# Optimization experiments

Measured on AMD Instinct MI355X. Metric: run time of the kernel, lower is better.

## Reference

```python
import jax, jax.numpy as jnp
import numpy as np

B, T, F = 256, 2048, 20
H_NODES = 256


def _heaviside(x):
    # smooth heaviside approx used throughout the original module
    return (jnp.tanh(10.0 * x) + 1.0) * 0.5


def _evap(wu, wl, wd, pet):
    h = _heaviside
    et1 = h(wu - pet) * pet + h(pet - wu) * wu
    rp = h(pet - et1) * (pet - et1)  # h(-(pet-et1))*0 term vanishes
    et22 = h(rp - wl) * wl + h(wl - rp) * rp
    et2 = h(rp) * et22
    et33 = h(rp - et2 - wd) * wd + h(wd - (rp - et2)) * (rp - et2)
    et3 = h(rp - et2) * et33
    return et1, et2, et3


def _runoff(wu, wl, wd, p, wum, wlm, wdm, b, c):
    wum = wum * 19.9 + 0.1
    wlm = wlm * 30.0 + 60.0
    wdm = wdm * 60.0 + 60.0
    c = c * 0.19 + 0.01
    b = b * 0.3 + 0.1
    w_total = wum + wlm + wdm
    s = c * (wu / w_total) ** 2 + b * (wl / w_total) ** 2
    return _heaviside(p - s) * (p - s)


def _partition(runoff, k1, k2, k3):
    k1 = k1 * 0.69 + 0.01
    k2 = k2 * 0.69 + 0.01
    k3 = k3 * 0.89 + 0.01
    sr = k1 * runoff
    itf = k2 * (runoff - sr)
    bf = k3 * (runoff - sr - itf)
    return sr, itf, bf


def setup_inputs() -> dict:
    key = jax.random.key(0)
    ks = jax.random.split(key, 7)
    u = lambda k, shp: jax.random.uniform(k, shp, jnp.float32, -0.05, 0.05)
    inputs = jax.random.uniform(ks[0], (B, T, F), jnp.float32)
    return {
        "inputs": inputs,
        "w1": u(ks[1], (15, H_NODES)),
        "b1": jnp.zeros((H_NODES,), jnp.float32),
        "w2": u(ks[2], (H_NODES, 64)),
        "b2": jnp.zeros((64,), jnp.float32),
        "w3": u(ks[3], (64, 8)),
        "b3": jnp.zeros((8,), jnp.float32),
    }


def reference(inputs, w1, b1, w2, b2, w3, b3):
    pet = inputs[..., 0:1]
    tmean = inputs[..., 1:2]
    p = inputs[..., 2:3]
    attrs = inputs[..., 5:]  # [B,T,15]

    # static-attribute -> physical-parameter MLP
    h1 = jnp.tanh(attrs @ w1 + b1)
    h2 = jnp.tanh(h1 @ w2 + b2)
    params = jax.nn.sigmoid(h2 @ w3 + b3)  # [B,T,8]

    xs = jnp.concatenate([pet, p, tmean, params], axis=-1)  # [B,T,11]

    def step(state, x):
        wu, wl, wd = state[:, 0:1], state[:, 1:2], state[:, 2:3]
        pet_t, p_t = x[:, 0:1], x[:, 1:2]
        et1, et2, et3 = _evap(wu, wl, wd, pet_t)
        clip = lambda d: jnp.clip(d, -1e5, 1e5)
        wu_n = wu + clip(p_t - et1)
        wl_n = wl + clip(p_t - et1 - et2)
        wd_n = wd + clip(p_t - et1 - et2 - et3)
        ns = jnp.concatenate([wu_n, wl_n, wd_n], axis=1)  # [B,3]
        return ns, ns

    init = jnp.zeros((inputs.shape[0], 3), inputs.dtype)
    _, outs = jax.lax.scan(step, init, jnp.swapaxes(xs, 0, 1))  # [T,B,3]
    outputs = jnp.swapaxes(outs, 0, 1)  # [B,T,3]

    wu, wl, wd = outputs[..., 0:1], outputs[..., 1:2], outputs[..., 2:3]
    wum, wlm, wdm = params[..., 0:1], params[..., 1:2], params[..., 2:3]
    b, c = params[..., 3:4], params[..., 4:5]
    k1, k2, k3 = params[..., 5:6], params[..., 6:7], params[..., 7:8]

    et1, et2, et3 = _evap(wu, wl, wd, pet)
    # NOTE: original call() swaps (wl,wd) and (wlm,wdm) here - kept faithful
    runoff = _runoff(wu, wd, wl, p, wum, wdm, wlm, b, c)
    sr, itf, bf = _partition(runoff, k1, k2, k3)
    total_q = sr + itf * 0.5 + bf * 0.25  # flow routing
    return total_q  # [B,T,1]
```

## Files before the change

### kernel.cpp

```cpp
#include <hip/hip_runtime.h>

#define B_ 256
#define T_ 2048
#define F_ 20
#define NT (B_*T_)
#define CH 16
#define NCH (T_/CH)

typedef __bf16 bf16x8 __attribute__((ext_vector_type(8)));
typedef float  f32x4  __attribute__((ext_vector_type(4)));

__device__ __forceinline__ float ex2(float x){ return __builtin_amdgcn_exp2f(x); }
__device__ __forceinline__ float rcpf_(float x){ return __builtin_amdgcn_rcpf(x); }

#define K10F 28.853900817779268f
#define K1F   2.8853900817779268f
#define LOG2E 1.4426950408889634f

__device__ __forceinline__ float hside(float x){ return 1.0f - rcpf_(ex2(K10F*x) + 1.0f); }
__device__ __forceinline__ float tanh_f(float z){ return 1.0f - 2.0f*rcpf_(ex2(K1F*z) + 1.0f); }
__device__ __forceinline__ float sigmoid_f(float z){ return rcpf_(1.0f + ex2(-LOG2E*z)); }


__global__ __launch_bounds__(256) void prep_kernel(const float* __restrict__ in,
                                                   float* __restrict__ ws){
  int r = blockIdx.x*256 + threadIdx.x;
  if (r >= NT) return;
  int b = r & (B_-1);
  int t = r >> 8;
  const float* src = in + ((size_t)b*T_ + t)*F_;
  ((float2*)ws)[r] = make_float2(src[0], src[2]);
}

__global__ __launch_bounds__(512) void fused_kernel(const float* __restrict__ in,
    const float* __restrict__ w1, const float* __restrict__ b1,
    const float* __restrict__ w2, const float* __restrict__ b2,
    const float* __restrict__ w3, const float* __restrict__ b3,
    float* __restrict__ ws){
  extern __shared__ char sm[];
  float* params = ws + 4*(size_t)NT;

  if (blockIdx.x < 4) {
    const float2* pp2 = (const float2*)ws;
    float* wuT = ws + 2*(size_t)NT;
    float* wdT = ws + 3*(size_t)NT;
    float*  d1L = (float*)sm;
    float*  bsQ = (float*)(sm + 8192);
    float2* rhL = (float2*)(sm + 24576);
    float2* qbL = (float2*)(sm + 40960);

    int tid = threadIdx.x;
    int wv = tid >> 6, lane = tid & 63;
    int boff = blockIdx.x * 64;

    float wu = 0.0f, wl = 0.0f, wd = 0.0f;
    float2 buf[2][8];

    if (wv == 0){
      #pragma unroll
      for (int g = 0; g < 2; ++g)
        #pragma unroll
        for (int i = 0; i < 8; ++i)
          buf[g][i] = pp2[(g*8 + i)*B_ + boff + lane];
    }

    for (int it = 0; it < NCH + 3; ++it){
      if (wv == 0){
        if (it < NCH){
          int c = it, par = c & 1;
          #pragma unroll
          for (int g = 0; g < 2; ++g){
            #pragma unroll
            for (int i = 0; i < 8; ++i){
              int s = g*8 + i;
              float pet = buf[g][i].x, p = buf[g][i].y;
              float d  = wu - pet;
              float r1 = rcpf_(ex2(K10F*d) + 1.0f);
              float d1 = -d*r1;
              float base = (p - pet) + d1;
              wu += base;
              wuT[(c*CH + s)*B_ + boff + lane] = wu;
              d1L[par*(CH*64) + s*64 + lane] = d1;
              bsQ[(c&3)*(CH*64) + s*64 + lane] = base;
            }
            int cn = (c + 1 < NCH) ? c + 1 : c;
            #pragma unroll
            for (int i = 0; i < 8; ++i)
              buf[g][i] = pp2[(cn*CH + g*8 + i)*B_ + boff + lane];
          }
        }
      } else if (wv == 1){
        if (it >= 1 && it <= NCH){
          int c = it - 1, par = c & 1;
          #pragma unroll
          for (int s = 0; s < CH; ++s){
            float d1 = d1L[par*(CH*64) + s*64 + lane];
            float r2 = rcpf_(ex2(K10F*d1) + 1.0f);
            float rp = fmaf(-d1, r2, d1);
            float hrp = 1.0f - rcpf_(ex2(K10F*rp) + 1.0f);
            rhL[par*(CH*64) + s*64 + lane] = make_float2(rp, hrp);
          }
        }
      } else if (wv == 2){
        if (it >= 2 && it <= NCH + 1){
          int c = it - 2, par = c & 1;
          #pragma unroll
          for (int s = 0; s < CH; ++s){
            float2 rh  = rhL[par*(CH*64) + s*64 + lane];
            float base = bsQ[(c&3)*(CH*64) + s*64 + lane];
            float d2   = rh.x - wl;
            float r    = rcpf_(ex2(K10F*d2) + 1.0f);
            float et22 = fmaf(d2, r, wl);
            float et2  = rh.y * et22;
            float b2   = base - et2;
            wl += b2;
            qbL[par*(CH*64) + s*64 + lane] = make_float2(rh.x - et2, b2);
          }
        }
      } else if (wv == 3){
        if (it >= 3){
          int c = it - 3, par = c & 1;
          #pragma unroll
          for (int s = 0; s < CH; ++s){
            float2 qb  = qbL[par*(CH*64) + s*64 + lane];
            float hqv  = 1.0f - rcpf_(ex2(K10F*qb.x) + 1.0f);
            float d3   = qb.x - wd;
            float r    = rcpf_(ex2(K10F*d3) + 1.0f);
            float et33 = fmaf(d3, r, wd);
            float et3  = hqv * et33;
            wd += qb.y - et3;
            wdT[(c*CH + s)*B_ + boff + lane] = wd;
          }
        }
      }
      __syncthreads();
    }
    return;
  }

  __bf16* w1f  = (__bf16*)sm;
  __bf16* w2f  = (__bf16*)(sm + 8192);
  float*  b1s  = (float*)(sm + 40960);
  float*  b2s  = (float*)(sm + 41984);
  float*  w3s  = (float*)(sm + 42240);
  float*  b3s  = (float*)(sm + 44288);
  __bf16* hbufA= (__bf16*)(sm + 44320);

  int tid = threadIdx.x;

  for (int s = tid; s < 16*32*8; s += 512) w1f[s] = (__bf16)0.0f;
  __syncthreads();
  for (int idx = tid; idx < 15*256; idx += 512){
    int k = idx >> 8, n = idx & 255;
    int ct = n >> 4;
    int l  = ((k>>3)*16) + (n & 15);
    int j  = k & 7;
    w1f[(ct*32 + l)*8 + j] = (__bf16)w1[idx];
  }
  for (int idx = tid; idx < 256*64; idx += 512){
    int k = idx >> 6, n = idx & 63;
    int kb = k >> 5;
    int lq = (k >> 3) & 3;
    int j  = k & 7;
    int ct = n >> 4;
    int l  = lq*16 + (n & 15);
    w2f[((kb*4 + ct)*64 + l)*8 + j] = (__bf16)w2[idx];
  }
  if (tid < 256) b1s[tid] = b1[tid];
  if (tid < 64)  b2s[tid] = b2[tid];
  if (tid < 512) w3s[tid] = w3[tid];
  if (tid < 8)   b3s[tid] = b3[tid];
  __syncthreads();

  int lane = tid & 63;
  int wv   = tid >> 6;
  int m    = lane & 15;
  int q    = lane >> 4;
  int r0   = (blockIdx.x - 4)*128 + wv*16;

  int rowA = r0 + m;
  int bA = rowA & (B_-1), tA = rowA >> 8;
  const float* ap = in + ((size_t)bA*T_ + tA)*F_ + 5;
  bf16x8 a1;
  #pragma unroll
  for (int j = 0; j < 8; ++j){
    int k = q*8 + j;
    float v = (k < 15) ? ap[k] : 0.0f;
    a1[j] = (__bf16)v;
  }

  __bf16* hb = hbufA + wv*1152;
  f32x4 zero4 = {0.0f, 0.0f, 0.0f, 0.0f};
  bf16x8 zero8;
  #pragma unroll
  for (int j = 0; j < 8; ++j) zero8[j] = (__bf16)0.0f;

  f32x4 acc2[4] = {zero4, zero4, zero4, zero4};

  #pragma unroll
  for (int p = 0; p < 4; ++p){
    #pragma unroll
    for (int c4 = 0; c4 < 4; ++c4){
      int ct = p*4 + c4;
      bf16x8 bw = zero8;
      if (lane < 32) bw = *(const bf16x8*)&w1f[(ct*32 + lane)*8];
      f32x4 c1 = __builtin_amdgcn_mfma_f32_16x16x32_bf16(a1, bw, zero4, 0, 0, 0);
      int f = c4*16 + m;
      float bb = b1s[p*64 + f];
      #pragma unroll
      for (int i = 0; i < 4; ++i){
        float h = tanh_f(c1[i] + bb);
        hb[(q*4 + i)*72 + f] = (__bf16)h;
      }
    }
    #pragma unroll
    for (int kb = 0; kb < 2; ++kb){
      bf16x8 a2 = *(const bf16x8*)&hb[m*72 + q*8 + kb*32];
      #pragma unroll
      for (int ct = 0; ct < 4; ++ct){
        bf16x8 bw2 = *(const bf16x8*)&w2f[(((p*2 + kb)*4 + ct)*64 + lane)*8];
        acc2[ct] = __builtin_amdgcn_mfma_f32_16x16x32_bf16(a2, bw2, acc2[ct], 0, 0, 0);
      }
    }
  }

  #pragma unroll
  for (int ct = 0; ct < 4; ++ct){
    int f = ct*16 + m;
    float bb = b2s[f];
    #pragma unroll
    for (int i = 0; i < 4; ++i){
      float h = tanh_f(acc2[ct][i] + bb);
      hb[(q*4 + i)*72 + f] = (__bf16)h;
    }
  }

  float z0 = b3s[2*q], z1 = b3s[2*q + 1];
  #pragma unroll
  for (int kb3 = 0; kb3 < 8; ++kb3){
    bf16x8 hv8 = *(const bf16x8*)&hb[m*72 + kb3*8];
    #pragma unroll
    for (int j = 0; j < 8; ++j){
      float hv = (float)hv8[j];
      int k = kb3*8 + j;
      z0 = fmaf(hv, w3s[k*8 + 2*q],     z0);
      z1 = fmaf(hv, w3s[k*8 + 2*q + 1], z1);
    }
  }
  int rowO = r0 + m;
  float2 outp = make_float2(sigmoid_f(z0), sigmoid_f(z1));
  *(float2*)&params[(size_t)rowO*8 + 2*q] = outp;
}

__global__ __launch_bounds__(256) void final_kernel(const float* __restrict__ ws,
                                                    float* __restrict__ out){
  int r = blockIdx.x*256 + threadIdx.x;
  if (r >= NT) return;
  const float2* pp2 = (const float2*)ws;
  const float* wuT  = ws + 2*(size_t)NT;
  const float* wdT  = ws + 3*(size_t)NT;
  const float* params = ws + 4*(size_t)NT;

  float p  = pp2[r].y;
  float wu = wuT[r], wd = wdT[r];
  const float4* pp = (const float4*)(params + (size_t)r*8);
  float4 p0 = pp[0], p1 = pp[1];
  float wum   = fmaf(p0.x, 19.9f, 0.1f);
  float wlm_s = fmaf(p0.z, 30.0f, 60.0f);
  float wdm_s = fmaf(p0.y, 60.0f, 60.0f);
  float cc = fmaf(p1.x, 0.19f, 0.01f);
  float bb = fmaf(p0.w, 0.30f, 0.10f);
  float wt = wum + wlm_s + wdm_s;
  float xu = wu / wt;
  float xd = wd / wt;
  float s  = cc*xu*xu + bb*xd*xd;
  float ps = p - s;
  float runoff = hside(ps)*ps;
  float k1p = fmaf(p1.y, 0.69f, 0.01f);
  float k2p = fmaf(p1.z, 0.69f, 0.01f);
  float k3p = fmaf(p1.w, 0.89f, 0.01f);
  float sr  = k1p*runoff;
  float itf = k2p*(runoff - sr);
  float bf  = k3p*(runoff - sr - itf);
  int b = r & (B_-1);
  int t = r >> 8;
  out[(size_t)b*T_ + t] = sr + 0.5f*itf + 0.25f*bf;
}

extern "C" void kernel_launch(void* const* d_in, const int* in_sizes, int n_in,
                              void* d_out, int out_size, void* d_ws, size_t ws_size,
                              hipStream_t stream) {
  const float* in = (const float*)d_in[0];
  const float* w1 = (const float*)d_in[1];
  const float* b1 = (const float*)d_in[2];
  const float* w2 = (const float*)d_in[3];
  const float* b2 = (const float*)d_in[4];
  const float* w3 = (const float*)d_in[5];
  const float* b3 = (const float*)d_in[6];
  float* out = (float*)d_out;
  float* ws  = (float*)d_ws;

  prep_kernel <<<NT/256,      256, 0,     stream>>>(in, ws);
  fused_kernel<<<NT/128 + 4,  512, 62752, stream>>>(in, w1, b1, w2, b2, w3, b3, ws);
  final_kernel<<<NT/256,      256, 0,     stream>>>(ws, out);
}
```

Before: 220.9 us.

## Split scan across more blocks, prescale state, offload loads/stores to helper waves

The serial scan now runs on 8 blocks of 32 lanes instead of 4 blocks of 64. Its state is kept pre-scaled by the tanh constant, which removes the multiply before each exp2. Global loads of the next chunk and global stores of wu/wd move to two extra helper waves that use shared-memory double buffers, so the latency-critical recurrence waves touch only LDS. The final kernel gains an LDS tile transpose so output stores are coalesced. The cost is half-empty wavefronts and an extra pipeline stage of latency.

```diff
diff --git a/kernel.cpp b/kernel.cpp
--- a/kernel.cpp
+++ b/kernel.cpp
@@ -14,6 +14,7 @@
 __device__ __forceinline__ float rcpf_(float x){ return __builtin_amdgcn_rcpf(x); }
 
 #define K10F 28.853900817779268f
+#define INVK 0.034657359027997264f
 #define K1F   2.8853900817779268f
 #define LOG2E 1.4426950408889634f
 
@@ -40,97 +41,130 @@
   extern __shared__ char sm[];
   float* params = ws + 4*(size_t)NT;
 
-  if (blockIdx.x < 4) {
+  if (blockIdx.x < 8) {
     const float2* pp2 = (const float2*)ws;
     float* wuT = ws + 2*(size_t)NT;
     float* wdT = ws + 3*(size_t)NT;
-    float*  d1L = (float*)sm;
-    float*  bsQ = (float*)(sm + 8192);
-    float2* rhL = (float2*)(sm + 24576);
-    float2* qbL = (float2*)(sm + 40960);
-
-    int tid = threadIdx.x;
-    int wv = tid >> 6, lane = tid & 63;
-    int boff = blockIdx.x * 64;
-
-    float wu = 0.0f, wl = 0.0f, wd = 0.0f;
-    float2 buf[2][8];
-
-    if (wv == 0){
+    float2* ppL = (float2*)sm;
+    float2* dkb = (float2*)(sm + 8192);
+    float2* rhb = (float2*)(sm + 16384);
+    float2* qbb = (float2*)(sm + 24576);
+    float*  bb2 = (float*)(sm + 32768);
+    float*  wub = (float*)(sm + 36864);
+    float*  wdb = (float*)(sm + 40960);
+
+    int tid  = threadIdx.x;
+    int wv   = tid >> 6;
+    int l64  = tid & 63;
+    bool act = l64 < 32;
+    int lane = l64 & 31;
+    int boff = blockIdx.x * 32;
+
+    float Wu = 0.0f, WL = 0.0f, WD = 0.0f;
+
+    if (wv == 4 && act){
+      float2 v[CH];
       #pragma unroll
-      for (int g = 0; g < 2; ++g)
-        #pragma unroll
-        for (int i = 0; i < 8; ++i)
-          buf[g][i] = pp2[(g*8 + i)*B_ + boff + lane];
-    }
-
-    for (int it = 0; it < NCH + 3; ++it){
+      for (int s = 0; s < CH; ++s) v[s] = pp2[s*B_ + boff + lane];
+      #pragma unroll
+      for (int s = 0; s < CH; ++s)
+        ppL[s*32 + lane] = make_float2(K10F*v[s].x, K10F*(v[s].y - v[s].x));
+    }
+    __syncthreads();
+
+    for (int it = 0; it < NCH + 4; ++it){
       if (wv == 0){
-        if (it < NCH){
-          int c = it, par = c & 1;
-          #pragma unroll
-          for (int g = 0; g < 2; ++g){
-            #pragma unroll
-            for (int i = 0; i < 8; ++i){
-              int s = g*8 + i;
-              float pet = buf[g][i].x, p = buf[g][i].y;
-              float d  = wu - pet;
-              float r1 = rcpf_(ex2(K10F*d) + 1.0f);
-              float d1 = -d*r1;
-              float base = (p - pet) + d1;
-              wu += base;
-              wuT[(c*CH + s)*B_ + boff + lane] = wu;
-              d1L[par*(CH*64) + s*64 + lane] = d1;
-              bsQ[(c&3)*(CH*64) + s*64 + lane] = base;
-            }
-            int cn = (c + 1 < NCH) ? c + 1 : c;
-            #pragma unroll
-            for (int i = 0; i < 8; ++i)
-              buf[g][i] = pp2[(cn*CH + g*8 + i)*B_ + boff + lane];
+        int c = it;
+        if (c < NCH && act){
+          int par = c & 1;
+          #pragma unroll
+          for (int s = 0; s < CH; ++s){
+            float2 pe = ppL[(par*CH + s)*32 + lane];
+            float t1  = Wu - pe.x;
+            float r   = rcpf_(ex2(t1) + 1.0f);
+            float WuPP= Wu + pe.y;
+            float Wn  = fmaf(-t1, r, WuPP);
+            float dK  = -t1*r;
+            float BASE= pe.y + dK;
+            dkb[(par*CH + s)*32 + lane] = make_float2(dK, BASE);
+            wub[(par*CH + s)*32 + lane] = Wn;
+            Wu = Wn;
           }
         }
       } else if (wv == 1){
-        if (it >= 1 && it <= NCH){
-          int c = it - 1, par = c & 1;
+        int c = it - 1;
+        if (c >= 0 && c < NCH && act){
+          int par = c & 1;
           #pragma unroll
           for (int s = 0; s < CH; ++s){
-            float d1 = d1L[par*(CH*64) + s*64 + lane];
-            float r2 = rcpf_(ex2(K10F*d1) + 1.0f);
-            float rp = fmaf(-d1, r2, d1);
-            float hrp = 1.0f - rcpf_(ex2(K10F*rp) + 1.0f);
-            rhL[par*(CH*64) + s*64 + lane] = make_float2(rp, hrp);
+            float2 db = dkb[(par*CH + s)*32 + lane];
+            float r1  = rcpf_(ex2(db.x) + 1.0f);
+            float RP  = fmaf(-db.x, r1, db.x);
+            float HRP = 1.0f - rcpf_(ex2(RP) + 1.0f);
+            rhb[(par*CH + s)*32 + lane] = make_float2(RP, HRP);
+            bb2[(par*CH + s)*32 + lane] = db.y;
           }
         }
       } else if (wv == 2){
-        if (it >= 2 && it <= NCH + 1){
-          int c = it - 2, par = c & 1;
+        int c = it - 2;
+        if (c >= 0 && c < NCH && act){
+          int par = c & 1;
           #pragma unroll
           for (int s = 0; s < CH; ++s){
-            float2 rh  = rhL[par*(CH*64) + s*64 + lane];
-            float base = bsQ[(c&3)*(CH*64) + s*64 + lane];
-            float d2   = rh.x - wl;
-            float r    = rcpf_(ex2(K10F*d2) + 1.0f);
-            float et22 = fmaf(d2, r, wl);
-            float et2  = rh.y * et22;
-            float b2   = base - et2;
-            wl += b2;
-            qbL[par*(CH*64) + s*64 + lane] = make_float2(rh.x - et2, b2);
+            float2 rh  = rhb[(par*CH + s)*32 + lane];
+            float BASE = bb2[(par*CH + s)*32 + lane];
+            float D2   = rh.x - WL;
+            float r    = rcpf_(ex2(D2) + 1.0f);
+            float et22 = fmaf(D2, r, WL);
+            float WLB  = WL + BASE;
+            float Wn   = fmaf(-rh.y, et22, WLB);
+            float ET2  = rh.y * et22;
+            qbb[(par*CH + s)*32 + lane] = make_float2(rh.x - ET2, BASE - ET2);
+            WL = Wn;
           }
         }
       } else if (wv == 3){
-        if (it >= 3){
-          int c = it - 3, par = c & 1;
+        int c = it - 3;
+        if (c >= 0 && c < NCH && act){
+          int par = c & 1;
           #pragma unroll
           for (int s = 0; s < CH; ++s){
-            float2 qb  = qbL[par*(CH*64) + s*64 + lane];
-            float hqv  = 1.0f - rcpf_(ex2(K10F*qb.x) + 1.0f);
-            float d3   = qb.x - wd;
-            float r    = rcpf_(ex2(K10F*d3) + 1.0f);
-            float et33 = fmaf(d3, r, wd);
-            float et3  = hqv * et33;
-            wd += qb.y - et3;
-            wdT[(c*CH + s)*B_ + boff + lane] = wd;
+            float2 qb  = qbb[(par*CH + s)*32 + lane];
+            float hqv  = 1.0f - rcpf_(ex2(qb.x) + 1.0f);
+            float D3   = qb.x - WD;
+            float r    = rcpf_(ex2(D3) + 1.0f);
+            float et33 = fmaf(D3, r, WD);
+            float WDB  = WD + qb.y;
+            float Wn   = fmaf(-hqv, et33, WDB);
+            wdb[(par*CH + s)*32 + lane] = Wn;
+            WD = Wn;
           }
+        }
+      } else if (wv == 4){
+        int cn = it + 1;
+        if (cn < NCH && act){
+          float2 v[CH];
+          #pragma unroll
+          for (int s = 0; s < CH; ++s) v[s] = pp2[(cn*CH + s)*B_ + boff + lane];
+          int par = cn & 1;
+          #pragma unroll
+          for (int s = 0; s < CH; ++s)
+            ppL[(par*CH + s)*32 + lane] = make_float2(K10F*v[s].x, K10F*(v[s].y - v[s].x));
+        }
+      } else if (wv == 5){
+        int cw = it - 1;
+        if (cw >= 0 && cw < NCH && act){
+          int par = cw & 1;
+          #pragma unroll
+          for (int s = 0; s < CH; ++s)
+            wuT[(cw*CH + s)*B_ + boff + lane] = wub[(par*CH + s)*32 + lane] * INVK;
+        }
+        int cd = it - 4;
+        if (cd >= 0 && cd < NCH && act){
+          int par = cd & 1;
+          #pragma unroll
+          for (int s = 0; s < CH; ++s)
+            wdT[(cd*CH + s)*B_ + boff + lane] = wdb[(par*CH + s)*32 + lane] * INVK;
         }
       }
       __syncthreads();
@@ -176,7 +210,7 @@
   int wv   = tid >> 6;
   int m    = lane & 15;
   int q    = lane >> 4;
-  int r0   = (blockIdx.x - 4)*128 + wv*16;
+  int r0   = (blockIdx.x - 8)*128 + wv*16;
 
   int rowA = r0 + m;
   int bA = rowA & (B_-1), tA = rowA >> 8;
@@ -254,37 +288,51 @@
 
 __global__ __launch_bounds__(256) void final_kernel(const float* __restrict__ ws,
                                                     float* __restrict__ out){
-  int r = blockIdx.x*256 + threadIdx.x;
-  if (r >= NT) return;
+  __shared__ float tile[64*65];
+  int tb = blockIdx.x & 31;
+  int bb = blockIdx.x >> 5;
+  int t0 = tb*64, b0 = bb*64;
+  int tid = threadIdx.x;
   const float2* pp2 = (const float2*)ws;
   const float* wuT  = ws + 2*(size_t)NT;
   const float* wdT  = ws + 3*(size_t)NT;
   const float* params = ws + 4*(size_t)NT;
 
-  float p  = pp2[r].y;
-  float wu = wuT[r], wd = wdT[r];
-  const float4* pp = (const float4*)(params + (size_t)r*8);
-  float4 p0 = pp[0], p1 = pp[1];
-  float wum   = fmaf(p0.x, 19.9f, 0.1f);
-  float wlm_s = fmaf(p0.z, 30.0f, 60.0f);
-  float wdm_s = fmaf(p0.y, 60.0f, 60.0f);
-  float cc = fmaf(p1.x, 0.19f, 0.01f);
-  float bb = fmaf(p0.w, 0.30f, 0.10f);
-  float wt = wum + wlm_s + wdm_s;
-  float xu = wu / wt;
-  float xd = wd / wt;
-  float s  = cc*xu*xu + bb*xd*xd;
-  float ps = p - s;
-  float runoff = hside(ps)*ps;
-  float k1p = fmaf(p1.y, 0.69f, 0.01f);
-  float k2p = fmaf(p1.z, 0.69f, 0.01f);
-  float k3p = fmaf(p1.w, 0.89f, 0.01f);
-  float sr  = k1p*runoff;
-  float itf = k2p*(runoff - sr);
-  float bf  = k3p*(runoff - sr - itf);
-  int b = r & (B_-1);
-  int t = r >> 8;
-  out[(size_t)b*T_ + t] = sr + 0.5f*itf + 0.25f*bf;
+  #pragma unroll
+  for (int k = 0; k < 16; ++k){
+    int idx = k*256 + tid;
+    int tl = idx >> 6, bl = idx & 63;
+    int r = (t0 + tl)*B_ + b0 + bl;
+    float p  = pp2[r].y;
+    float wu = wuT[r], wd = wdT[r];
+    const float4* pp = (const float4*)(params + (size_t)r*8);
+    float4 p0 = pp[0], p1 = pp[1];
+    float wum   = fmaf(p0.x, 19.9f, 0.1f);
+    float wlm_s = fmaf(p0.z, 30.0f, 60.0f);
+    float wdm_s = fmaf(p0.y, 60.0f, 60.0f);
+    float cc = fmaf(p1.x, 0.19f, 0.01f);
+    float bcoef = fmaf(p0.w, 0.30f, 0.10f);
+    float wt = wum + wlm_s + wdm_s;
+    float xu = wu / wt;
+    float xd = wd / wt;
+    float s  = cc*xu*xu + bcoef*xd*xd;
+    float ps = p - s;
+    float runoff = hside(ps)*ps;
+    float k1p = fmaf(p1.y, 0.69f, 0.01f);
+    float k2p = fmaf(p1.z, 0.69f, 0.01f);
+    float k3p = fmaf(p1.w, 0.89f, 0.01f);
+    float sr  = k1p*runoff;
+    float itf = k2p*(runoff - sr);
+    float bf  = k3p*(runoff - sr - itf);
+    tile[bl*65 + tl] = sr + 0.5f*itf + 0.25f*bf;
+  }
+  __syncthreads();
+  #pragma unroll
+  for (int k = 0; k < 16; ++k){
+    int idx = k*256 + tid;
+    int tl2 = idx & 63, bl2 = idx >> 6;
+    out[(size_t)(b0 + bl2)*T_ + t0 + tl2] = tile[bl2*65 + tl2];
+  }
 }
 
 extern "C" void kernel_launch(void* const* d_in, const int* in_sizes, int n_in,
@@ -301,6 +349,6 @@
   float* ws  = (float*)d_ws;
 
   prep_kernel <<<NT/256,      256, 0,     stream>>>(in, ws);
-  fused_kernel<<<NT/128 + 4,  512, 62752, stream>>>(in, w1, b1, w2, b2, w3, b3, ws);
-  final_kernel<<<NT/256,      256, 0,     stream>>>(ws, out);
+  fused_kernel<<<NT/128 + 8,  512, 62752, stream>>>(in, w1, b1, w2, b2, w3, b3, ws);
+  final_kernel<<<128,         256, 0,     stream>>>(ws, out);
 }
```

Result: slower. 229.7 us (+4.0%).

## Fold param transforms into MLP epilogue, transpose final output via LDS, prioritize scan

Applied to the files above, without the earlier changes.

The MLP epilogue now folds the eight sigmoid parameters into three per-row coefficients (runoff quadratic weights and a combined partition gain), stored as a float4 instead of eight floats. This halves the params traffic and removes divisions from the final kernel. The final kernel now processes 64x64 tiles and transposes through shared memory, so output writes are coalesced along T instead of strided. It also adds s_setprio on the scan blocks so they get scheduling priority while running concurrently with the MLP blocks.

```diff
diff --git a/kernel.cpp b/kernel.cpp
--- a/kernel.cpp
+++ b/kernel.cpp
@@ -38,9 +38,10 @@
     const float* __restrict__ w3, const float* __restrict__ b3,
     float* __restrict__ ws){
   extern __shared__ char sm[];
-  float* params = ws + 4*(size_t)NT;
+  float* pk4 = ws + 4*(size_t)NT;
 
   if (blockIdx.x < 4) {
+    asm volatile("s_setprio 3");
     const float2* pp2 = (const float2*)ws;
     float* wuT = ws + 2*(size_t)NT;
     float* wdT = ws + 3*(size_t)NT;
@@ -247,44 +248,62 @@
       z1 = fmaf(hv, w3s[k*8 + 2*q + 1], z1);
     }
   }
-  int rowO = r0 + m;
-  float2 outp = make_float2(sigmoid_f(z0), sigmoid_f(z1));
-  *(float2*)&params[(size_t)rowO*8 + 2*q] = outp;
+
+  float* hf = (float*)hb;
+  hf[m*8 + 2*q]     = sigmoid_f(z0);
+  hf[m*8 + 2*q + 1] = sigmoid_f(z1);
+  if (q == 0){
+    float P0=hf[m*8+0], P1=hf[m*8+1], P2=hf[m*8+2], P3=hf[m*8+3];
+    float P4=hf[m*8+4], P5=hf[m*8+5], P6=hf[m*8+6], P7=hf[m*8+7];
+    float wum = fmaf(P0, 19.9f, 0.1f);
+    float wlm = fmaf(P2, 30.0f, 60.0f);
+    float wdm = fmaf(P1, 60.0f, 60.0f);
+    float wt  = wum + wlm + wdm;
+    float rw  = 1.0f / wt;
+    float cc  = fmaf(P4, 0.19f, 0.01f);
+    float bc  = fmaf(P3, 0.30f, 0.10f);
+    float A   = cc*rw*rw;
+    float Bc  = bc*rw*rw;
+    float k1  = fmaf(P5, 0.69f, 0.01f);
+    float k2  = fmaf(P6, 0.69f, 0.01f);
+    float k3  = fmaf(P7, 0.89f, 0.01f);
+    float KP  = k1 + 0.5f*k2*(1.0f-k1) + 0.25f*k3*(1.0f-k1)*(1.0f-k2);
+    int rowO = r0 + m;
+    *(float4*)&pk4[(size_t)rowO*4] = make_float4(A, Bc, KP, 0.0f);
+  }
 }
 
 __global__ __launch_bounds__(256) void final_kernel(const float* __restrict__ ws,
                                                     float* __restrict__ out){
-  int r = blockIdx.x*256 + threadIdx.x;
-  if (r >= NT) return;
+  __shared__ float tile[64*65];
+  int tb = blockIdx.x & 31;
+  int bb = blockIdx.x >> 5;
+  int t0 = tb*64, b0 = bb*64;
+  int tid = threadIdx.x;
   const float2* pp2 = (const float2*)ws;
   const float* wuT  = ws + 2*(size_t)NT;
   const float* wdT  = ws + 3*(size_t)NT;
-  const float* params = ws + 4*(size_t)NT;
-
-  float p  = pp2[r].y;
-  float wu = wuT[r], wd = wdT[r];
-  const float4* pp = (const float4*)(params + (size_t)r*8);
-  float4 p0 = pp[0], p1 = pp[1];
-  float wum   = fmaf(p0.x, 19.9f, 0.1f);
-  float wlm_s = fmaf(p0.z, 30.0f, 60.0f);
-  float wdm_s = fmaf(p0.y, 60.0f, 60.0f);
-  float cc = fmaf(p1.x, 0.19f, 0.01f);
-  float bb = fmaf(p0.w, 0.30f, 0.10f);
-  float wt = wum + wlm_s + wdm_s;
-  float xu = wu / wt;
-  float xd = wd / wt;
-  float s  = cc*xu*xu + bb*xd*xd;
-  float ps = p - s;
-  float runoff = hside(ps)*ps;
-  float k1p = fmaf(p1.y, 0.69f, 0.01f);
-  float k2p = fmaf(p1.z, 0.69f, 0.01f);
-  float k3p = fmaf(p1.w, 0.89f, 0.01f);
-  float sr  = k1p*runoff;
-  float itf = k2p*(runoff - sr);
-  float bf  = k3p*(runoff - sr - itf);
-  int b = r & (B_-1);
-  int t = r >> 8;
-  out[(size_t)b*T_ + t] = sr + 0.5f*itf + 0.25f*bf;
+  const float* pk4  = ws + 4*(size_t)NT;
+
+  #pragma unroll
+  for (int k = 0; k < 16; ++k){
+    int idx = k*256 + tid;
+    int tl = idx >> 6, bl = idx & 63;
+    int r = (t0 + tl)*B_ + b0 + bl;
+    float p  = pp2[r].y;
+    float wu = wuT[r], wd = wdT[r];
+    float4 k4 = *(const float4*)&pk4[(size_t)r*4];
+    float ps = p - k4.x*wu*wu - k4.y*wd*wd;
+    float runoff = hside(ps)*ps;
+    tile[bl*65 + tl] = k4.z * runoff;
+  }
+  __syncthreads();
+  #pragma unroll
+  for (int k = 0; k < 16; ++k){
+    int idx = k*256 + tid;
+    int tl2 = idx & 63, bl2 = idx >> 6;
+    out[(size_t)(b0 + bl2)*T_ + t0 + tl2] = tile[bl2*65 + tl2];
+  }
 }
 
 extern "C" void kernel_launch(void* const* d_in, const int* in_sizes, int n_in,
@@ -300,7 +319,7 @@
   float* out = (float*)d_out;
   float* ws  = (float*)d_ws;
 
-  prep_kernel <<<NT/256,      256, 0,     stream>>>(in, ws);
-  fused_kernel<<<NT/128 + 4,  512, 62752, stream>>>(in, w1, b1, w2, b2, w3, b3, ws);
-  final_kernel<<<NT/256,      256, 0,     stream>>>(ws, out);
+  prep_kernel <<<NT/256,     256, 0,     stream>>>(in, ws);
+  fused_kernel<<<NT/128 + 4, 512, 62752, stream>>>(in, w1, b1, w2, b2, w3, b3, ws);
+  final_kernel<<<128,        256, 0,     stream>>>(ws, out);
 }
```

New measurement: 218.6 us. No clear change (-1.0%).
